# Kernel tuning notes

Measured on AMD Instinct MI355X. Metric: run time of the kernel, lower is better.

The kernel has to match this reference:

```python
import jax, jax.numpy as jnp
import numpy as np

EPS = 1e-12  # torch F.normalize default eps


def _nn_idx(q, ref):
    # q: [P,3], ref: [M,3] -> nearest-ref index per query point (brute-force chamfer NN)
    d = (jnp.sum(q * q, axis=-1, keepdims=True)
         - 2.0 * (q @ ref.T)
         + jnp.sum(ref * ref, axis=-1))  # [P,M]
    return jnp.argmin(d, axis=-1)  # [P]


def _verts_normals(verts, faces):
    # verts: [N,3], faces: [F,3] int. Area-weighted vertex normals (pytorch3d style):
    # accumulate the face cross-product into each incident vertex.
    v0 = verts[faces[:, 0]]
    v1 = verts[faces[:, 1]]
    v2 = verts[faces[:, 2]]
    fn = jnp.cross(v1 - v0, v2 - v0)  # [F,3], magnitude = 2*area
    n = jnp.zeros_like(verts)
    n = n.at[faces[:, 0]].add(fn)
    n = n.at[faces[:, 1]].add(fn)
    n = n.at[faces[:, 2]].add(fn)
    return n  # [N,3] (unnormalized; normalized downstream)


def _normalize(x):
    nrm = jnp.linalg.norm(x, axis=-1, keepdims=True)
    return x / jnp.maximum(nrm, EPS)


def setup_inputs() -> dict:
    key = jax.random.key(0)
    k1, k2, k3, k4 = jax.random.split(key, 4)
    B, P, V, N, F = 8, 2048, 2562, 8192, 16384
    return {
        "pred_points": jax.random.normal(k1, (B, P, 3), dtype=jnp.float32),
        "pred_vertices": jax.random.normal(k2, (B, V, 3), dtype=jnp.float32),
        "gt_vertices": jax.random.normal(k3, (B, N, 3), dtype=jnp.float32),
        "gt_faces": jax.random.randint(k4, (B, F, 3), 0, N, dtype=jnp.int64),
    }


def reference(pred_points, pred_vertices, gt_vertices, gt_faces):
    # nearest gt vertex for every sampled pred point (per-batch chamfer NN)
    nearest_gt_idx = jax.vmap(_nn_idx)(pred_points, gt_vertices)       # [B,P]
    # nearest pred-mesh vertex for every sampled pred point
    nearest_pred_idx = jax.vmap(_nn_idx)(pred_points, pred_vertices)   # [B,P]

    # gather nearest pred vertices: [B,P,3]
    nearest_pred_vertices = jnp.take_along_axis(
        pred_vertices, nearest_pred_idx[..., None], axis=1)

    # gt vertex normals, gathered at nearest gt indices, then normalized
    gt_normals = jax.vmap(_verts_normals)(gt_vertices, gt_faces)       # [B,N,3]
    nearest_gt_normals = jnp.take_along_axis(
        gt_normals, nearest_gt_idx[..., None], axis=1)                 # [B,P,3]
    nearest_gt_normals = _normalize(nearest_gt_normals)

    # edge from nearest pred vertex to sampled point, normalized
    nearest_pred_edges = _normalize(pred_points - nearest_pred_vertices)

    normal_loss = jnp.mean(jnp.abs(
        jnp.sum(nearest_pred_edges * nearest_gt_normals, axis=2)))
    return normal_loss
```

## Files before the change

### kernel.cpp

```cpp
#include <hip/hip_runtime.h>
#include <math.h>

#define BB 8
#define PP 2048
#define VV 2562
#define NV 8192
#define FF 16384
#define EPSF 1e-12f
#define NSLICE 4
#define FSLICE (FF / NSLICE)

__global__ __launch_bounds__(1024) void face_normals_kernel(
    const float* __restrict__ gtv,
    const int*   __restrict__ faces,
    float*       __restrict__ nrm)
{
    __shared__ float acc[NV * 3];
    const int b = blockIdx.x >> 2;
    const int s = blockIdx.x & 3;

    for (int i = threadIdx.x; i < NV * 3; i += 1024) acc[i] = 0.f;
    __syncthreads();

    const int*   fb = faces + ((size_t)b * FF + (size_t)s * FSLICE) * 3;
    const float* vb = gtv   + (size_t)b * NV * 3;

    for (int f = threadIdx.x; f < FSLICE; f += 1024) {
        int i0 = fb[f*3+0], i1 = fb[f*3+1], i2 = fb[f*3+2];

        float v0x = vb[i0*3+0], v0y = vb[i0*3+1], v0z = vb[i0*3+2];
        float v1x = vb[i1*3+0], v1y = vb[i1*3+1], v1z = vb[i1*3+2];
        float v2x = vb[i2*3+0], v2y = vb[i2*3+1], v2z = vb[i2*3+2];

        float e1x = v1x - v0x, e1y = v1y - v0y, e1z = v1z - v0z;
        float e2x = v2x - v0x, e2y = v2y - v0y, e2z = v2z - v0z;

        float fnx = e1y * e2z - e1z * e2y;
        float fny = e1z * e2x - e1x * e2z;
        float fnz = e1x * e2y - e1y * e2x;

        atomicAdd(&acc[i0*3+0], fnx); atomicAdd(&acc[i0*3+1], fny); atomicAdd(&acc[i0*3+2], fnz);
        atomicAdd(&acc[i1*3+0], fnx); atomicAdd(&acc[i1*3+1], fny); atomicAdd(&acc[i1*3+2], fnz);
        atomicAdd(&acc[i2*3+0], fnx); atomicAdd(&acc[i2*3+1], fny); atomicAdd(&acc[i2*3+2], fnz);
    }
    __syncthreads();

    float* nb = nrm + (size_t)b * NV * 3;
    for (int i = threadIdx.x; i < NV * 3; i += 1024) atomicAdd(&nb[i], acc[i]);
}

__global__ __launch_bounds__(256) void nn_loss_kernel(
    const float* __restrict__ pp,
    const float* __restrict__ pv,
    const float* __restrict__ gtv,
    const float* __restrict__ nrm,
    float*       __restrict__ out)
{
    const int lane = threadIdx.x & 63;
    const int wave = threadIdx.x >> 6;
    const int gw   = blockIdx.x * 4 + wave;
    const int b    = gw >> 9;
    const int p0   = (gw & 511) * 4;

    float px[4], py[4], pz[4], m2x[4], m2y[4], m2z[4];
    const float* ppb = pp + ((size_t)b * PP + p0) * 3;
#pragma unroll
    for (int j = 0; j < 4; ++j) {
        px[j] = ppb[j*3+0]; py[j] = ppb[j*3+1]; pz[j] = ppb[j*3+2];
        m2x[j] = -2.f * px[j]; m2y[j] = -2.f * py[j]; m2z[j] = -2.f * pz[j];
    }

    float bd[4]; int bi[4];

#pragma unroll
    for (int j = 0; j < 4; ++j) { bd[j] = INFINITY; bi[j] = 0; }
    const float* gvb = gtv + (size_t)b * NV * 3;
    for (int i = 0; i < NV / 64; ++i) {
        int r = lane + i * 64;
        float rx = gvb[r*3+0], ry = gvb[r*3+1], rz = gvb[r*3+2];
        float rr = fmaf(rx, rx, fmaf(ry, ry, rz * rz));
#pragma unroll
        for (int j = 0; j < 4; ++j) {
            float s = fmaf(m2x[j], rx, fmaf(m2y[j], ry, fmaf(m2z[j], rz, rr)));
            bool take = s < bd[j];
            bd[j] = take ? s : bd[j];
            bi[j] = take ? r : bi[j];
        }
    }
    int gt_idx[4];
#pragma unroll
    for (int j = 0; j < 4; ++j) {
        float d = bd[j]; int idx = bi[j];
#pragma unroll
        for (int off = 32; off; off >>= 1) {
            float od = __shfl_xor(d, off);
            int   oi = __shfl_xor(idx, off);
            if (od < d || (od == d && oi < idx)) { d = od; idx = oi; }
        }
        gt_idx[j] = idx;
    }

#pragma unroll
    for (int j = 0; j < 4; ++j) { bd[j] = INFINITY; bi[j] = 0; }
    const float* pvb = pv + (size_t)b * VV * 3;
    for (int i = 0; i < (VV + 63) / 64; ++i) {
        int r = lane + i * 64;
        bool ok = r < VV;
        int rc = ok ? r : 0;
        float rx = pvb[rc*3+0], ry = pvb[rc*3+1], rz = pvb[rc*3+2];
        float rr = fmaf(rx, rx, fmaf(ry, ry, rz * rz));
#pragma unroll
        for (int j = 0; j < 4; ++j) {
            float s = fmaf(m2x[j], rx, fmaf(m2y[j], ry, fmaf(m2z[j], rz, rr)));
            s = ok ? s : INFINITY;
            bool take = s < bd[j];
            bd[j] = take ? s : bd[j];
            bi[j] = take ? r : bi[j];
        }
    }
    int pr_idx[4];
#pragma unroll
    for (int j = 0; j < 4; ++j) {
        float d = bd[j]; int idx = bi[j];
#pragma unroll
        for (int off = 32; off; off >>= 1) {
            float od = __shfl_xor(d, off);
            int   oi = __shfl_xor(idx, off);
            if (od < d || (od == d && oi < idx)) { d = od; idx = oi; }
        }
        pr_idx[j] = idx;
    }

    __shared__ float wsum[4];
    if (lane == 0) {
        const float* nb = nrm + (size_t)b * NV * 3;
        float s = 0.f;
#pragma unroll
        for (int j = 0; j < 4; ++j) {
            int vi = pr_idx[j];
            float ex = px[j] - pvb[vi*3+0];
            float ey = py[j] - pvb[vi*3+1];
            float ez = pz[j] - pvb[vi*3+2];
            float el = fmaxf(sqrtf(fmaf(ex, ex, fmaf(ey, ey, ez * ez))), EPSF);

            int ni = gt_idx[j];
            float nx = nb[ni*3+0];
            float ny = nb[ni*3+1];
            float nz = nb[ni*3+2];
            float nl = fmaxf(sqrtf(fmaf(nx, nx, fmaf(ny, ny, nz * nz))), EPSF);

            float dot = fmaf(ex, nx, fmaf(ey, ny, ez * nz));
            s += fabsf(dot) / (el * nl);
        }
        wsum[wave] = s;
    }
    __syncthreads();
    if (threadIdx.x == 0)
        atomicAdd(out, (wsum[0] + wsum[1] + wsum[2] + wsum[3]) *
                       (1.f / (float)(BB * PP)));
}

extern "C" void kernel_launch(void* const* d_in, const int* in_sizes, int n_in,
                              void* d_out, int out_size, void* d_ws, size_t ws_size,
                              hipStream_t stream) {
    const float* pp    = (const float*)d_in[0];
    const float* pv    = (const float*)d_in[1];
    const float* gtv   = (const float*)d_in[2];
    const int*   faces = (const int*)d_in[3];
    float* out = (float*)d_out;

    float* nrm = (float*)d_ws;

    hipMemsetAsync(nrm, 0, (size_t)BB * NV * 3 * sizeof(float), stream);
    hipMemsetAsync(out, 0, sizeof(float), stream);

    face_normals_kernel<<<BB * NSLICE, 1024, 0, stream>>>(gtv, faces, nrm);

    nn_loss_kernel<<<(BB * PP) / 16, 256, 0, stream>>>(pp, pv, gtv, nrm, out);
}
```

Before: 162.9 us.

## Stage NN reference points in double-buffered LDS tiles and store per-slice normal partials

The nearest-neighbour kernel now cooperatively loads the gt and pred vertex arrays into double-buffered shared-memory tiles, instead of every wave reading them from global memory. The next tile is prefetched into registers while the current one is scanned. The face-normal kernel uses twice as many slices and writes per-slice partial sums rather than global atomics, so the memset is dropped. The loss kernel sums the partials at the gathered index. The tiling adds block-wide barriers, and reading the partials costs extra gathers (eight slices per normal).

```diff
diff --git a/kernel.cpp b/kernel.cpp
--- a/kernel.cpp
+++ b/kernel.cpp
@@ -7,17 +7,18 @@
 #define NV 8192
 #define FF 16384
 #define EPSF 1e-12f
-#define NSLICE 4
+#define NSLICE 8
 #define FSLICE (FF / NSLICE)
+#define TS 512
 
 __global__ __launch_bounds__(1024) void face_normals_kernel(
     const float* __restrict__ gtv,
     const int*   __restrict__ faces,
-    float*       __restrict__ nrm)
+    float*       __restrict__ part)
 {
     __shared__ float acc[NV * 3];
-    const int b = blockIdx.x >> 2;
-    const int s = blockIdx.x & 3;
+    const int b = blockIdx.x >> 3;
+    const int s = blockIdx.x & 7;
 
     for (int i = threadIdx.x; i < NV * 3; i += 1024) acc[i] = 0.f;
     __syncthreads();
@@ -45,19 +46,23 @@
     }
     __syncthreads();
 
-    float* nb = nrm + (size_t)b * NV * 3;
-    for (int i = threadIdx.x; i < NV * 3; i += 1024) atomicAdd(&nb[i], acc[i]);
+    float* pb = part + ((size_t)b * NSLICE + s) * (NV * 3);
+    for (int i = threadIdx.x; i < NV * 3; i += 1024) pb[i] = acc[i];
 }
 
 __global__ __launch_bounds__(256) void nn_loss_kernel(
     const float* __restrict__ pp,
     const float* __restrict__ pv,
     const float* __restrict__ gtv,
-    const float* __restrict__ nrm,
+    const float* __restrict__ part,
     float*       __restrict__ out)
 {
-    const int lane = threadIdx.x & 63;
-    const int wave = threadIdx.x >> 6;
+    __shared__ float tile[2][TS * 3];
+    __shared__ float wsum[4];
+
+    const int tid  = threadIdx.x;
+    const int lane = tid & 63;
+    const int wave = tid >> 6;
     const int gw   = blockIdx.x * 4 + wave;
     const int b    = gw >> 9;
     const int p0   = (gw & 511) * 4;
@@ -74,17 +79,44 @@
 
 #pragma unroll
     for (int j = 0; j < 4; ++j) { bd[j] = INFINITY; bi[j] = 0; }
-    const float* gvb = gtv + (size_t)b * NV * 3;
-    for (int i = 0; i < NV / 64; ++i) {
-        int r = lane + i * 64;
-        float rx = gvb[r*3+0], ry = gvb[r*3+1], rz = gvb[r*3+2];
-        float rr = fmaf(rx, rx, fmaf(ry, ry, rz * rz));
-#pragma unroll
-        for (int j = 0; j < 4; ++j) {
-            float s = fmaf(m2x[j], rx, fmaf(m2y[j], ry, fmaf(m2z[j], rz, rr)));
-            bool take = s < bd[j];
-            bd[j] = take ? s : bd[j];
-            bi[j] = take ? r : bi[j];
+    {
+        const float* gsrc = gtv + (size_t)b * NV * 3;
+#pragma unroll
+        for (int k = 0; k < 6; ++k)
+            tile[0][tid + k * 256] = gsrc[tid + k * 256];
+        __syncthreads();
+
+        for (int t = 0; t < NV / TS; ++t) {
+            const int cur = t & 1, nxt = cur ^ 1;
+            const bool have_next = (t + 1) < (NV / TS);
+            float g[6];
+            if (have_next) {
+#pragma unroll
+                for (int k = 0; k < 6; ++k)
+                    g[k] = gsrc[(t + 1) * (TS * 3) + tid + k * 256];
+            }
+#pragma unroll 2
+            for (int i = 0; i < TS / 64; ++i) {
+                int r = lane + i * 64;
+                float rx = tile[cur][r*3+0];
+                float ry = tile[cur][r*3+1];
+                float rz = tile[cur][r*3+2];
+                float rr = fmaf(rx, rx, fmaf(ry, ry, rz * rz));
+                int rg = t * TS + r;
+#pragma unroll
+                for (int j = 0; j < 4; ++j) {
+                    float sc = fmaf(m2x[j], rx, fmaf(m2y[j], ry, fmaf(m2z[j], rz, rr)));
+                    bool take = sc < bd[j];
+                    bd[j] = take ? sc : bd[j];
+                    bi[j] = take ? rg : bi[j];
+                }
+            }
+            if (have_next) {
+#pragma unroll
+                for (int k = 0; k < 6; ++k)
+                    tile[nxt][tid + k * 256] = g[k];
+            }
+            __syncthreads();
         }
     }
     int gt_idx[4];
@@ -102,20 +134,49 @@
 
 #pragma unroll
     for (int j = 0; j < 4; ++j) { bd[j] = INFINITY; bi[j] = 0; }
-    const float* pvb = pv + (size_t)b * VV * 3;
-    for (int i = 0; i < (VV + 63) / 64; ++i) {
-        int r = lane + i * 64;
-        bool ok = r < VV;
-        int rc = ok ? r : 0;
-        float rx = pvb[rc*3+0], ry = pvb[rc*3+1], rz = pvb[rc*3+2];
-        float rr = fmaf(rx, rx, fmaf(ry, ry, rz * rz));
-#pragma unroll
-        for (int j = 0; j < 4; ++j) {
-            float s = fmaf(m2x[j], rx, fmaf(m2y[j], ry, fmaf(m2z[j], rz, rr)));
-            s = ok ? s : INFINITY;
-            bool take = s < bd[j];
-            bd[j] = take ? s : bd[j];
-            bi[j] = take ? r : bi[j];
+    {
+        const float* psrc = pv + (size_t)b * VV * 3;
+        const int NT = (VV + TS - 1) / TS;
+#pragma unroll
+        for (int k = 0; k < 6; ++k)
+            tile[0][tid + k * 256] = psrc[tid + k * 256];
+        __syncthreads();
+
+        for (int t = 0; t < NT; ++t) {
+            const int cur = t & 1, nxt = cur ^ 1;
+            const bool have_next = (t + 1) < NT;
+            float g[6];
+            if (have_next) {
+#pragma unroll
+                for (int k = 0; k < 6; ++k) {
+                    int gi = (t + 1) * (TS * 3) + tid + k * 256;
+                    g[k] = (gi < VV * 3) ? psrc[gi] : 0.f;
+                }
+            }
+            const int nt = (VV - t * TS < TS) ? (VV - t * TS) : TS;
+            for (int i = 0; i < (nt + 63) / 64; ++i) {
+                int r = lane + i * 64;
+                bool ok = r < nt;
+                float rx = tile[cur][r*3+0];
+                float ry = tile[cur][r*3+1];
+                float rz = tile[cur][r*3+2];
+                float rr = fmaf(rx, rx, fmaf(ry, ry, rz * rz));
+                int rg = t * TS + r;
+#pragma unroll
+                for (int j = 0; j < 4; ++j) {
+                    float sc = fmaf(m2x[j], rx, fmaf(m2y[j], ry, fmaf(m2z[j], rz, rr)));
+                    sc = ok ? sc : INFINITY;
+                    bool take = sc < bd[j];
+                    bd[j] = take ? sc : bd[j];
+                    bi[j] = take ? rg : bi[j];
+                }
+            }
+            if (have_next) {
+#pragma unroll
+                for (int k = 0; k < 6; ++k)
+                    tile[nxt][tid + k * 256] = g[k];
+            }
+            __syncthreads();
         }
     }
     int pr_idx[4];
@@ -131,9 +192,9 @@
         pr_idx[j] = idx;
     }
 
-    __shared__ float wsum[4];
     if (lane == 0) {
-        const float* nb = nrm + (size_t)b * NV * 3;
+        const float* pvb = pv + (size_t)b * VV * 3;
+        const float* pt0 = part + (size_t)b * NSLICE * (NV * 3);
         float s = 0.f;
 #pragma unroll
         for (int j = 0; j < 4; ++j) {
@@ -144,9 +205,12 @@
             float el = fmaxf(sqrtf(fmaf(ex, ex, fmaf(ey, ey, ez * ez))), EPSF);
 
             int ni = gt_idx[j];
-            float nx = nb[ni*3+0];
-            float ny = nb[ni*3+1];
-            float nz = nb[ni*3+2];
+            float nx = 0.f, ny = 0.f, nz = 0.f;
+#pragma unroll
+            for (int sl = 0; sl < NSLICE; ++sl) {
+                const float* pb = pt0 + (size_t)sl * (NV * 3) + (size_t)ni * 3;
+                nx += pb[0]; ny += pb[1]; nz += pb[2];
+            }
             float nl = fmaxf(sqrtf(fmaf(nx, nx, fmaf(ny, ny, nz * nz))), EPSF);
 
             float dot = fmaf(ex, nx, fmaf(ey, ny, ez * nz));
@@ -155,7 +219,7 @@
         wsum[wave] = s;
     }
     __syncthreads();
-    if (threadIdx.x == 0)
+    if (tid == 0)
         atomicAdd(out, (wsum[0] + wsum[1] + wsum[2] + wsum[3]) *
                        (1.f / (float)(BB * PP)));
 }
@@ -169,12 +233,11 @@
     const int*   faces = (const int*)d_in[3];
     float* out = (float*)d_out;
 
-    float* nrm = (float*)d_ws;
-
-    hipMemsetAsync(nrm, 0, (size_t)BB * NV * 3 * sizeof(float), stream);
+    float* part = (float*)d_ws;
+
     hipMemsetAsync(out, 0, sizeof(float), stream);
 
-    face_normals_kernel<<<BB * NSLICE, 1024, 0, stream>>>(gtv, faces, nrm);
-
-    nn_loss_kernel<<<(BB * PP) / 16, 256, 0, stream>>>(pp, pv, gtv, nrm, out);
+    face_normals_kernel<<<BB * NSLICE, 1024, 0, stream>>>(gtv, faces, part);
+
+    nn_loss_kernel<<<(BB * PP) / 16, 256, 0, stream>>>(pp, pv, gtv, part, out);
 }
```

Result: slower. 183.0 us (+12.4%).
